# Kernel optimization log

Hardware: AMD Instinct MI355X
Metric: run time of the kernel (lower is better)

## Reference

```python
import jax, jax.numpy as jnp
import numpy as np

B, V, T = 8, 16, 64
DIN, H, RH, K, TMP = 6, 256, 64, 2, 256
E = V * (V - 1)
NREL, NPOS = 7, 3  # 2D relative / positional feature counts

_edges = np.ones((V, V)) - np.eye(V)
SEND = jnp.asarray(np.where(_edges)[0])
RECV = jnp.asarray(np.where(_edges)[1])


def _w(k, shape, fan):
    return jax.random.normal(k, shape, jnp.float32) / np.sqrt(fan)


def setup_inputs() -> dict:
    key = jax.random.key(0)
    ks = jax.random.split(key, 20)
    d = {}
    d['rel_feat'] = jax.random.normal(ks[0], (B, V, T, DIN), jnp.float32)
    d['edge_attr_raw'] = jax.random.normal(ks[1], (B, E, T, NREL + DIN), jnp.float32)
    d['edge_pos'] = jax.random.normal(ks[2], (B, E, T, NPOS), jnp.float32)
    d['ef_w1'] = _w(ks[3], (H, NREL + DIN + NPOS), NREL + DIN + NPOS); d['ef_b1'] = jnp.full((H,), 0.1)
    d['ef_w2'] = _w(ks[4], (H, H), H); d['ef_b2'] = jnp.full((H,), 0.1)
    d['res_w'] = _w(ks[5], (H, DIN), DIN); d['res_b'] = jnp.full((H,), 0.1)
    d['m3_w1'] = _w(ks[6], (H, H), H); d['m3_b1'] = jnp.full((H,), 0.1)
    d['m3_w2'] = _w(ks[7], (H, H), H); d['m3_b2'] = jnp.full((H,), 0.1)
    d['m4_w1'] = _w(ks[8], (H, 3 * H), 3 * H); d['m4_b1'] = jnp.full((H,), 0.1)
    d['m4_w2'] = _w(ks[9], (H, H), H); d['m4_b2'] = jnp.full((H,), 0.1)
    d['f_wih'] = _w(ks[10], (4 * RH, H), H); d['f_whh'] = _w(ks[11], (4 * RH, RH), RH)
    d['f_bih'] = jnp.zeros((4 * RH,)); d['f_bhh'] = jnp.zeros((4 * RH,))
    d['r_wih'] = _w(ks[12], (4 * RH, H), H); d['r_whh'] = _w(ks[13], (4 * RH, RH), RH)
    d['r_bih'] = jnp.zeros((4 * RH,)); d['r_bhh'] = jnp.zeros((4 * RH,))
    d['p_w'] = _w(ks[14], (K, RH), RH); d['p_b'] = jnp.full((K,), 0.1)
    d['e_w1'] = _w(ks[15], (TMP, 2 * RH), 2 * RH); d['e_b1'] = jnp.full((TMP,), 0.1)
    d['e_w2'] = _w(ks[16], (K, TMP), TMP); d['e_b2'] = jnp.full((K,), 0.1)
    return d


def _lstm(x, wih, whh, bih, bhh):
    # x: [N, T, H] -> hidden sequence [N, T, RH]; torch gate order i, f, g, o
    n = x.shape[0]
    rh = whh.shape[1]
    xw = jnp.einsum('nth,gh->ntg', x, wih) + bih  # input GEMM hoisted out of scan

    def step(carry, xt):
        h, c = carry
        z = xt + h @ whh.T + bhh
        i, f, g, o = jnp.split(z, 4, axis=-1)
        c = jax.nn.sigmoid(f) * c + jax.nn.sigmoid(i) * jnp.tanh(g)
        h = jax.nn.sigmoid(o) * jnp.tanh(c)
        return (h, c), h

    h0 = jnp.zeros((n, rh), x.dtype)
    _, hs = jax.lax.scan(step, (h0, h0), jnp.swapaxes(xw, 0, 1))
    return jnp.swapaxes(hs, 0, 1)


def reference(rel_feat, edge_attr_raw, edge_pos, ef_w1, ef_b1, ef_w2, ef_b2, res_w, res_b, m3_w1, m3_b1, m3_w2, m3_b2, m4_w1, m4_b1, m4_w2, m4_b2, f_wih, f_whh, f_bih, f_bhh, r_wih, r_whh, r_bih, r_bhh, p_w, p_b, e_w1, e_b1, e_w2, e_b2):
    elu = jax.nn.elu
    # edge filter MLP: [B,E,T,NREL+DIN+NPOS] -> [B,E,T,H]
    ein = jnp.concatenate([edge_attr_raw, edge_pos], -1)
    edge_attr = elu(elu(ein @ ef_w1.T + ef_b1) @ ef_w2.T + ef_b2)
    # edge2node: scatter-sum over recv indices, normalized by (V-1)
    agg = jax.ops.segment_sum(jnp.moveaxis(edge_attr, 1, 0), RECV, num_segments=V)
    x = jnp.moveaxis(agg, 0, 1) / (V - 1) + (rel_feat @ res_w.T + res_b)
    # mlp3 on node embeddings
    x = elu(elu(x @ m3_w1.T + m3_b1) @ m3_w2.T + m3_b2)
    # node2edge gather + skip-concat with previous edge features -> mlp4
    x = jnp.concatenate([x[:, SEND], x[:, RECV], edge_attr], -1)  # [B,E,T,3H]
    x = elu(elu(x @ m4_w1.T + m4_b1) @ m4_w2.T + m4_b2)  # [B,E,T,H]
    # bidirectional LSTM over time, per edge
    seq = x.reshape(B * E, T, H)
    fwd = _lstm(seq, f_wih, f_whh, f_bih, f_bhh)
    rev = jnp.flip(_lstm(jnp.flip(seq, 1), r_wih, r_whh, r_bih, r_bhh), 1)
    prior = (fwd @ p_w.T + p_b).reshape(B, E, T, K).transpose(0, 2, 1, 3)  # [B,T,E,K]
    comb = jnp.concatenate([fwd, rev], -1)
    enc = (elu(comb @ e_w1.T + e_b1) @ e_w2.T + e_b2).reshape(B, E, T, K).transpose(0, 2, 1, 3)
    return prior, enc
```

## Files before the change

kernel.cpp:

```cpp
#include <hip/hip_runtime.h>
#include <cstdint>
#include <cstddef>
#include <type_traits>

#define B_ 8
#define V_ 16
#define T_ 64
#define E_ 240
#define H_ 256
#define RH_ 64
#define K_ 2
#define DIN_ 6
#define BET_ (B_*E_*T_)
#define BVT_ (B_*V_*T_)
#define BE_ (B_*E_)

typedef unsigned short ushort_t;
typedef unsigned int u32;
typedef __attribute__((ext_vector_type(8))) short bf16x8;
typedef __attribute__((ext_vector_type(4))) float f32x4;

__device__ __forceinline__ float eluf(float x) { return x > 0.f ? x : __expf(x) - 1.f; }
__device__ __forceinline__ float fsig(float x) { return 1.f / (1.f + __expf(-x)); }
__device__ __forceinline__ float ftanh_(float x) {
    float y = fminf(fmaxf(x, -8.f), 8.f);
    float e = __expf(2.f * y);
    return (e - 1.f) / (e + 1.f);
}
__device__ __forceinline__ float b2f(ushort_t u) {
    union { float f; uint32_t i; } v; v.i = ((uint32_t)u) << 16; return v.f;
}
__device__ __forceinline__ ushort_t f2b(float f) {
    union { float f; uint32_t i; } v; v.f = f;
    uint32_t r = (v.i + 0x7FFFu + ((v.i >> 16) & 1u)) >> 16;
    return (ushort_t)r;
}

__device__ __forceinline__ void gll16(const void* g, void* l) {
    __builtin_amdgcn_global_load_lds(
        (const __attribute__((address_space(1))) u32*)g,
        (__attribute__((address_space(3))) u32*)l, 16, 0, 0);
}

template<int KD, int ACT>
__global__ __launch_bounds__(512, 2) void gemm8_k(
    const ushort_t* __restrict__ A, const ushort_t* __restrict__ Wt,
    const float* __restrict__ b1, const float* __restrict__ b2,
    ushort_t* __restrict__ C)
{
    __shared__ ushort_t lds[4][32][512];
    const int tid = threadIdx.x;
    const int lane = tid & 63;
    const int w = tid >> 6;
    const int wm = w >> 2, wn = w & 3;
    const int m0 = blockIdx.x * 256;
    const int r16 = lane & 15, kq = lane >> 4;
    constexpr int NH = KD / 32;

    const ushort_t* Ag0 = A + (size_t)(m0 + w * 16 + r16) * KD + kq * 8;
    const ushort_t* Ag1 = A + (size_t)(m0 + (w + 8) * 16 + r16) * KD + kq * 8;
    const ushort_t* Bg0 = Wt + (size_t)(w * 16 + r16) * KD + kq * 8;
    const ushort_t* Bg1 = Wt + (size_t)((w + 8) * 16 + r16) * KD + kq * 8;

    f32x4 acc[8][4];
    #pragma unroll
    for (int i = 0; i < 8; ++i)
        #pragma unroll
        for (int j = 0; j < 4; ++j)
            acc[i][j] = (f32x4){0.f, 0.f, 0.f, 0.f};

#define ST8(h) do { int sl_ = (h) & 3; int kk_ = (h) * 32;                  \
    gll16(Ag0 + kk_, &lds[sl_][w][0]);                                      \
    gll16(Ag1 + kk_, &lds[sl_][w + 8][0]);                                  \
    gll16(Bg0 + kk_, &lds[sl_][16 + w][0]);                                 \
    gll16(Bg1 + kk_, &lds[sl_][16 + w + 8][0]);                             \
} while (0)

    ST8(0); ST8(1); ST8(2);
    asm volatile("s_waitcnt vmcnt(8)" ::: "memory");
    __builtin_amdgcn_s_barrier();

    for (int h = 0; h < NH; ++h) {
        if (h + 3 < NH) ST8(h + 3);
        const int sl = h & 3;
        bf16x8 bfr[4];
        #pragma unroll
        for (int nf = 0; nf < 4; ++nf)
            bfr[nf] = *(const bf16x8*)&lds[sl][16 + wn * 4 + nf][lane * 8];
        #pragma unroll
        for (int mh = 0; mh < 2; ++mh) {
            bf16x8 af[4];
            #pragma unroll
            for (int mf = 0; mf < 4; ++mf)
                af[mf] = *(const bf16x8*)&lds[sl][wm * 8 + mh * 4 + mf][lane * 8];
            __builtin_amdgcn_s_setprio(1);
            #pragma unroll
            for (int mf = 0; mf < 4; ++mf)
                #pragma unroll
                for (int nf = 0; nf < 4; ++nf)
                    acc[mh * 4 + mf][nf] = __builtin_amdgcn_mfma_f32_16x16x32_bf16(
                        bfr[nf], af[mf], acc[mh * 4 + mf][nf], 0, 0, 0);
            __builtin_amdgcn_s_setprio(0);
        }
        asm volatile("s_waitcnt lgkmcnt(0)" ::: "memory");
        if (h < NH - 3)       { asm volatile("s_waitcnt vmcnt(8)" ::: "memory"); }
        else if (h == NH - 3) { asm volatile("s_waitcnt vmcnt(4)" ::: "memory"); }
        else if (h == NH - 2) { asm volatile("s_waitcnt vmcnt(0)" ::: "memory"); }
        if (h < NH - 1) __builtin_amdgcn_s_barrier();
    }
#undef ST8

    #pragma unroll
    for (int mi = 0; mi < 8; ++mi) {
        int mrow = m0 + wm * 128 + mi * 16 + r16;
        #pragma unroll
        for (int nf = 0; nf < 4; ++nf) {
            int nb = wn * 64 + nf * 16 + kq * 4;
            float4 bb = *(const float4*)&b1[nb];
            if (b2) {
                float4 b2v = *(const float4*)&b2[nb];
                bb.x += b2v.x; bb.y += b2v.y; bb.z += b2v.z; bb.w += b2v.w;
            }
            float v0 = acc[mi][nf][0] + bb.x;
            float v1 = acc[mi][nf][1] + bb.y;
            float v2 = acc[mi][nf][2] + bb.z;
            float v3 = acc[mi][nf][3] + bb.w;
            if (ACT) { v0 = eluf(v0); v1 = eluf(v1); v2 = eluf(v2); v3 = eluf(v3); }
            ushort4 o; o.x = f2b(v0); o.y = f2b(v1); o.z = f2b(v2); o.w = f2b(v3);
            *(ushort4*)&C[(size_t)mrow * 256 + nb] = o;
        }
    }
}

__global__ __launch_bounds__(512, 1) void gemm8_ef_k(
    const float* __restrict__ ear, const float* __restrict__ epos,
    const float* __restrict__ ef_w1, const float* __restrict__ ef_b1,
    const ushort_t* __restrict__ w_ef2, const float* __restrict__ ef_b2,
    ushort_t* __restrict__ EA)
{
    __shared__ ushort_t H1[8][8][512];
    __shared__ ushort_t slotB[4][16][512];
    const int tid = threadIdx.x;
    const int lane = tid & 63;
    const int w = tid >> 6;
    const int wm = w >> 2, wn = w & 3;
    const int m0 = blockIdx.x * 128;
    const int r16 = lane & 15, kq = lane >> 4;

    f32x4 acc[4][4];
    #pragma unroll
    for (int i = 0; i < 4; ++i)
        #pragma unroll
        for (int j = 0; j < 4; ++j)
            acc[i][j] = (f32x4){0.f, 0.f, 0.f, 0.f};
    {
        bf16x8 af[4], bfr[4];
        #pragma unroll
        for (int mf = 0; mf < 4; ++mf) {
            int m = m0 + wm * 64 + mf * 16 + r16;
            #pragma unroll
            for (int e = 0; e < 8; ++e) {
                float v = 0.f;
                if (kq < 2) {
                    int c = kq * 8 + e;
                    v = (c < 13) ? ear[(size_t)m * 13 + c] : epos[(size_t)m * 3 + (c - 13)];
                }
                af[mf][e] = (short)f2b(v);
            }
        }
        #pragma unroll
        for (int nf = 0; nf < 4; ++nf) {
            int n = wn * 64 + nf * 16 + r16;
            #pragma unroll
            for (int e = 0; e < 8; ++e) {
                float v = 0.f;
                if (kq < 2) v = ef_w1[(size_t)n * 16 + kq * 8 + e];
                bfr[nf][e] = (short)f2b(v);
            }
        }
        #pragma unroll
        for (int mf = 0; mf < 4; ++mf)
            #pragma unroll
            for (int nf = 0; nf < 4; ++nf)
                acc[mf][nf] = __builtin_amdgcn_mfma_f32_16x16x32_bf16(bfr[nf], af[mf], acc[mf][nf], 0, 0, 0);
    }

    const size_t bo0 = (size_t)(2 * w * 16 + r16) * 256 + kq * 8;
    const size_t bo1 = (size_t)((2 * w + 1) * 16 + r16) * 256 + kq * 8;
#define EF_ST(h) do { int sl_ = (h) & 3;                                    \
    gll16(w_ef2 + bo0 + (h) * 32, &slotB[sl_][2 * w][0]);                   \
    gll16(w_ef2 + bo1 + (h) * 32, &slotB[sl_][2 * w + 1][0]);               \
} while (0)

    EF_ST(0); EF_ST(1); EF_ST(2);

    #pragma unroll
    for (int mf = 0; mf < 4; ++mf) {
        #pragma unroll
        for (int nf = 0; nf < 4; ++nf) {
            int col = wn * 64 + nf * 16 + kq * 4;
            float4 bb = *(const float4*)&ef_b1[col];
            ushort4 o;
            o.x = f2b(eluf(acc[mf][nf][0] + bb.x));
            o.y = f2b(eluf(acc[mf][nf][1] + bb.y));
            o.z = f2b(eluf(acc[mf][nf][2] + bb.z));
            o.w = f2b(eluf(acc[mf][nf][3] + bb.w));
            int ktw = wn * 2 + (nf >> 1);
            int lanew = r16 + 16 * (((nf & 1) << 1) | (kq >> 1));
            *(ushort4*)&H1[wm * 4 + mf][ktw][lanew * 8 + (kq & 1) * 4] = o;
            acc[mf][nf] = (f32x4){0.f, 0.f, 0.f, 0.f};
        }
    }
    asm volatile("s_waitcnt lgkmcnt(0)" ::: "memory");
    asm volatile("s_waitcnt vmcnt(4)" ::: "memory");
    __builtin_amdgcn_s_barrier();

    #pragma unroll
    for (int h = 0; h < 8; ++h) {
        if (h + 3 < 8) EF_ST(h + 3);
        const int sl = h & 3;
        bf16x8 af[4], bfr[4];
        #pragma unroll
        for (int nf = 0; nf < 4; ++nf)
            bfr[nf] = *(const bf16x8*)&slotB[sl][wn * 4 + nf][lane * 8];
        #pragma unroll
        for (int mf = 0; mf < 4; ++mf)
            af[mf] = *(const bf16x8*)&H1[wm * 4 + mf][h][lane * 8];
        __builtin_amdgcn_s_setprio(1);
        #pragma unroll
        for (int mf = 0; mf < 4; ++mf)
            #pragma unroll
            for (int nf = 0; nf < 4; ++nf)
                acc[mf][nf] = __builtin_amdgcn_mfma_f32_16x16x32_bf16(bfr[nf], af[mf], acc[mf][nf], 0, 0, 0);
        __builtin_amdgcn_s_setprio(0);
        asm volatile("s_waitcnt lgkmcnt(0)" ::: "memory");
        if (h <= 4)      { asm volatile("s_waitcnt vmcnt(4)" ::: "memory"); }
        else if (h == 5) { asm volatile("s_waitcnt vmcnt(2)" ::: "memory"); }
        else if (h == 6) { asm volatile("s_waitcnt vmcnt(0)" ::: "memory"); }
        if (h < 7) __builtin_amdgcn_s_barrier();
    }
#undef EF_ST

    #pragma unroll
    for (int mf = 0; mf < 4; ++mf) {
        int row = m0 + wm * 64 + mf * 16 + r16;
        #pragma unroll
        for (int nf = 0; nf < 4; ++nf) {
            int col = wn * 64 + nf * 16 + kq * 4;
            float4 bb = *(const float4*)&ef_b2[col];
            ushort4 o;
            o.x = f2b(eluf(acc[mf][nf][0] + bb.x));
            o.y = f2b(eluf(acc[mf][nf][1] + bb.y));
            o.z = f2b(eluf(acc[mf][nf][2] + bb.z));
            o.w = f2b(eluf(acc[mf][nf][3] + bb.w));
            *(ushort4*)&EA[(size_t)row * 256 + col] = o;
        }
    }
}

__global__ __launch_bounds__(512, 1) void gemm8_mlp3_k(
    const ushort_t* __restrict__ Xb, const ushort_t* __restrict__ w1,
    const float* __restrict__ b1, const ushort_t* __restrict__ w2,
    const float* __restrict__ b2, ushort_t* __restrict__ Out)
{
    __shared__ ushort_t H1[8][8][512];
    __shared__ ushort_t slots[36864];
    const int tid = threadIdx.x;
    const int lane = tid & 63;
    const int w = tid >> 6;
    const int m0 = blockIdx.x * 128;
    const int r16 = lane & 15, kq = lane >> 4;

    const ushort_t* Ag = Xb + (size_t)(m0 + w * 16 + r16) * 256 + kq * 8;
    const size_t bo0 = (size_t)(2 * w * 16 + r16) * 256 + kq * 8;
    const size_t bo1 = (size_t)((2 * w + 1) * 16 + r16) * 256 + kq * 8;

    float4 bb1[2], bb2[2];
    #pragma unroll
    for (int nf = 0; nf < 2; ++nf) {
        bb1[nf] = *(const float4*)&b1[w * 32 + nf * 16 + kq * 4];
        bb2[nf] = *(const float4*)&b2[w * 32 + nf * 16 + kq * 4];
    }

#define M3_ST0(h) do { int sl_ = (h) % 3;                                   \
    gll16(Ag + (h) * 32, &slots[sl_ * 12288 + w * 512]);                    \
    gll16(w1 + bo0 + (h) * 32, &slots[sl_ * 12288 + 4096 + 2 * w * 512]);   \
    gll16(w1 + bo1 + (h) * 32, &slots[sl_ * 12288 + 4096 + (2 * w + 1) * 512]); \
} while (0)
#define M3_ST1(h) do { int sl_ = (h) & 1; int kk_ = (h) * 32;               \
    gll16(w2 + bo0 + kk_, &slots[sl_ * 8192 + 2 * w * 512]);                \
    gll16(w2 + bo1 + kk_, &slots[sl_ * 8192 + (2 * w + 1) * 512]);          \
} while (0)

    f32x4 acc0[8][2];
    #pragma unroll
    for (int i = 0; i < 8; ++i) { acc0[i][0] = (f32x4){0,0,0,0}; acc0[i][1] = (f32x4){0,0,0,0}; }

    M3_ST0(0); M3_ST0(1);
    asm volatile("s_waitcnt vmcnt(3)" ::: "memory");
    __builtin_amdgcn_s_barrier();

    for (int h = 0; h < 8; ++h) {
        if (h + 2 < 8) M3_ST0(h + 2);
        const int sl = h % 3;
        bf16x8 af[8], bfr[2];
        #pragma unroll
        for (int mf = 0; mf < 8; ++mf)
            af[mf] = *(const bf16x8*)&slots[sl * 12288 + mf * 512 + lane * 8];
        #pragma unroll
        for (int nf = 0; nf < 2; ++nf)
            bfr[nf] = *(const bf16x8*)&slots[sl * 12288 + 4096 + (2 * w + nf) * 512 + lane * 8];
        #pragma unroll
        for (int mf = 0; mf < 8; ++mf)
            #pragma unroll
            for (int nf = 0; nf < 2; ++nf)
                acc0[mf][nf] = __builtin_amdgcn_mfma_f32_16x16x32_bf16(bfr[nf], af[mf], acc0[mf][nf], 0, 0, 0);
        asm volatile("s_waitcnt lgkmcnt(0)" ::: "memory");
        if (h <= 5)      { asm volatile("s_waitcnt vmcnt(3)" ::: "memory"); }
        else if (h == 6) { asm volatile("s_waitcnt vmcnt(0)" ::: "memory"); }
        if (h < 7) __builtin_amdgcn_s_barrier();
    }

    M3_ST1(0);
    #pragma unroll
    for (int mf = 0; mf < 8; ++mf) {
        #pragma unroll
        for (int nf = 0; nf < 2; ++nf) {
            ushort4 o;
            o.x = f2b(eluf(acc0[mf][nf][0] + bb1[nf].x));
            o.y = f2b(eluf(acc0[mf][nf][1] + bb1[nf].y));
            o.z = f2b(eluf(acc0[mf][nf][2] + bb1[nf].z));
            o.w = f2b(eluf(acc0[mf][nf][3] + bb1[nf].w));
            int lanew = r16 + 16 * ((nf << 1) | (kq >> 1));
            *(ushort4*)&H1[mf][w][lanew * 8 + (kq & 1) * 4] = o;
            acc0[mf][nf] = (f32x4){0.f, 0.f, 0.f, 0.f};
        }
    }
    asm volatile("s_waitcnt lgkmcnt(0)" ::: "memory");
    asm volatile("s_waitcnt vmcnt(0)" ::: "memory");
    __builtin_amdgcn_s_barrier();

    for (int h = 0; h < 8; ++h) {
        if (h + 1 < 8) M3_ST1(h + 1);
        const int sl = h & 1;
        bf16x8 af[8], bfr[2];
        #pragma unroll
        for (int mf = 0; mf < 8; ++mf)
            af[mf] = *(const bf16x8*)&H1[mf][h][lane * 8];
        #pragma unroll
        for (int nf = 0; nf < 2; ++nf)
            bfr[nf] = *(const bf16x8*)&slots[sl * 8192 + (2 * w + nf) * 512 + lane * 8];
        #pragma unroll
        for (int mf = 0; mf < 8; ++mf)
            #pragma unroll
            for (int nf = 0; nf < 2; ++nf)
                acc0[mf][nf] = __builtin_amdgcn_mfma_f32_16x16x32_bf16(bfr[nf], af[mf], acc0[mf][nf], 0, 0, 0);
        asm volatile("s_waitcnt lgkmcnt(0)" ::: "memory");
        if (h + 1 < 8) { asm volatile("s_waitcnt vmcnt(0)" ::: "memory"); }
        if (h < 7) __builtin_amdgcn_s_barrier();
    }

    #pragma unroll
    for (int mf = 0; mf < 8; ++mf) {
        int row = m0 + mf * 16 + r16;
        #pragma unroll
        for (int nf = 0; nf < 2; ++nf) {
            int col = w * 32 + nf * 16 + kq * 4;
            ushort4 o;
            o.x = f2b(eluf(acc0[mf][nf][0] + bb2[nf].x));
            o.y = f2b(eluf(acc0[mf][nf][1] + bb2[nf].y));
            o.z = f2b(eluf(acc0[mf][nf][2] + bb2[nf].z));
            o.w = f2b(eluf(acc0[mf][nf][3] + bb2[nf].w));
            *(ushort4*)&Out[(size_t)row * 256 + col] = o;
        }
    }
#undef M3_ST0
#undef M3_ST1
}

__global__ __launch_bounds__(512, 2) void gemm8_mlp4_k(
    const ushort_t* __restrict__ X2b, const ushort_t* __restrict__ EA,
    const ushort_t* __restrict__ Wt, const float* __restrict__ b1,
    ushort_t* __restrict__ C)
{
    __shared__ ushort_t lds[4][32][512];
    const int tid = threadIdx.x;
    const int lane = tid & 63;
    const int w = tid >> 6;
    const int wm = w >> 2, wn = w & 3;
    const int m0 = blockIdx.x * 256;
    const int r16 = lane & 15, kq = lane >> 4;
    constexpr int NH = 24;

    const ushort_t* AS[2]; const ushort_t* AR[2]; const ushort_t* AE[2];
    #pragma unroll
    for (int ff = 0; ff < 2; ++ff) {
        int f = w + ff * 8;
        int m = m0 + f * 16 + r16;
        int be = m >> 6, t = m & 63;
        int b = be / E_, e = be % E_;
        int s = e / (V_ - 1);
        int r0 = e % (V_ - 1);
        int rr = r0 + (r0 >= s ? 1 : 0);
        AS[ff] = X2b + ((size_t)((b * V_ + s) * T_ + t)) * H_ + kq * 8;
        AR[ff] = X2b + ((size_t)((b * V_ + rr) * T_ + t)) * H_ + kq * 8;
        AE[ff] = EA + (size_t)m * H_ + kq * 8;
    }
    const ushort_t* Bg0 = Wt + (size_t)(w * 16 + r16) * 768 + kq * 8;
    const ushort_t* Bg1 = Wt + (size_t)((w + 8) * 16 + r16) * 768 + kq * 8;

    f32x4 acc[8][4];
    #pragma unroll
    for (int i = 0; i < 8; ++i)
        #pragma unroll
        for (int j = 0; j < 4; ++j)
            acc[i][j] = (f32x4){0.f, 0.f, 0.f, 0.f};

#define STM(h) do { int sl_ = (h) & 3; int kk_ = (h) * 32;                  \
    int seg_ = kk_ >> 8, off_ = kk_ & 255;                                  \
    const ushort_t* a0_ = (seg_ == 0 ? AS[0] : seg_ == 1 ? AR[0] : AE[0]) + off_; \
    const ushort_t* a1_ = (seg_ == 0 ? AS[1] : seg_ == 1 ? AR[1] : AE[1]) + off_; \
    gll16(a0_, &lds[sl_][w][0]);                                            \
    gll16(a1_, &lds[sl_][w + 8][0]);                                        \
    gll16(Bg0 + kk_, &lds[sl_][16 + w][0]);                                 \
    gll16(Bg1 + kk_, &lds[sl_][16 + w + 8][0]);                             \
} while (0)

    STM(0); STM(1); STM(2);
    asm volatile("s_waitcnt vmcnt(8)" ::: "memory");
    __builtin_amdgcn_s_barrier();

    for (int h = 0; h < NH; ++h) {
        if (h + 3 < NH) STM(h + 3);
        const int sl = h & 3;
        bf16x8 bfr[4];
        #pragma unroll
        for (int nf = 0; nf < 4; ++nf)
            bfr[nf] = *(const bf16x8*)&lds[sl][16 + wn * 4 + nf][lane * 8];
        #pragma unroll
        for (int mh = 0; mh < 2; ++mh) {
            bf16x8 af[4];
            #pragma unroll
            for (int mf = 0; mf < 4; ++mf)
                af[mf] = *(const bf16x8*)&lds[sl][wm * 8 + mh * 4 + mf][lane * 8];
            __builtin_amdgcn_s_setprio(1);
            #pragma unroll
            for (int mf = 0; mf < 4; ++mf)
                #pragma unroll
                for (int nf = 0; nf < 4; ++nf)
                    acc[mh * 4 + mf][nf] = __builtin_amdgcn_mfma_f32_16x16x32_bf16(
                        bfr[nf], af[mf], acc[mh * 4 + mf][nf], 0, 0, 0);
            __builtin_amdgcn_s_setprio(0);
        }
        asm volatile("s_waitcnt lgkmcnt(0)" ::: "memory");
        if (h < NH - 3)       { asm volatile("s_waitcnt vmcnt(8)" ::: "memory"); }
        else if (h == NH - 3) { asm volatile("s_waitcnt vmcnt(4)" ::: "memory"); }
        else if (h == NH - 2) { asm volatile("s_waitcnt vmcnt(0)" ::: "memory"); }
        if (h < NH - 1) __builtin_amdgcn_s_barrier();
    }
#undef STM

    #pragma unroll
    for (int mi = 0; mi < 8; ++mi) {
        int mrow = m0 + wm * 128 + mi * 16 + r16;
        #pragma unroll
        for (int nf = 0; nf < 4; ++nf) {
            int nb = wn * 64 + nf * 16 + kq * 4;
            float4 bb = *(const float4*)&b1[nb];
            float v0 = eluf(acc[mi][nf][0] + bb.x);
            float v1 = eluf(acc[mi][nf][1] + bb.y);
            float v2 = eluf(acc[mi][nf][2] + bb.z);
            float v3 = eluf(acc[mi][nf][3] + bb.w);
            ushort4 o; o.x = f2b(v0); o.y = f2b(v1); o.z = f2b(v2); o.w = f2b(v3);
            *(ushort4*)&C[(size_t)mrow * 256 + nb] = o;
        }
    }
}

__global__ __launch_bounds__(256) void wconv_k(
    const float* __restrict__ ef_w2, const float* __restrict__ m4_w1,
    const float* __restrict__ m4_w2, const float* __restrict__ f_wih,
    const float* __restrict__ r_wih, const float* __restrict__ e_w1,
    const float* __restrict__ m3_w1, const float* __restrict__ m3_w2,
    ushort_t* __restrict__ Wb)
{
    int i = blockIdx.x * 256 + threadIdx.x;
    const float* src; int off;
    if (i < 65536)       { src = ef_w2; off = i; }
    else if (i < 262144) { src = m4_w1; off = i - 65536; }
    else if (i < 327680) { src = m4_w2; off = i - 262144; }
    else if (i < 393216) { src = f_wih; off = i - 327680; }
    else if (i < 458752) { src = r_wih; off = i - 393216; }
    else if (i < 491520) { src = e_w1;  off = i - 458752; }
    else if (i < 557056) { src = m3_w1; off = i - 491520; }
    else                 { src = m3_w2; off = i - 557056; }
    Wb[i] = f2b(src[off]);
}

__global__ __launch_bounds__(256) void e2n_k(
    const ushort_t* __restrict__ EA, const float* __restrict__ rel,
    const float* __restrict__ res_w, const float* __restrict__ res_b,
    ushort_t* __restrict__ X)
{
    const int idx = blockIdx.x;
    const int t = idx & (T_ - 1);
    const int bv = idx >> 6;
    const int v = bv & (V_ - 1);
    const int b = bv >> 4;
    const int h = threadIdx.x;
    float sum = 0.f;
    #pragma unroll
    for (int i = 0; i < V_; ++i) {
        if (i == v) continue;
        int jj = (v < i) ? v : v - 1;
        int e = i * (V_ - 1) + jj;
        sum += b2f(EA[(((size_t)(b * E_ + e)) * T_ + t) * H_ + h]);
    }
    const float* rp = rel + ((size_t)bv * T_ + t) * DIN_;
    float res = res_b[h];
    #pragma unroll
    for (int d = 0; d < DIN_; ++d) res += rp[d] * res_w[h * DIN_ + d];
    X[((size_t)bv * T_ + t) * H_ + h] = f2b(sum * (1.f / 15.f) + res);
}

__global__ __launch_bounds__(256) void lstm_mfma4_k(
    const ushort_t* __restrict__ Gf, const ushort_t* __restrict__ Gr,
    const float* __restrict__ whh_f, const float* __restrict__ whh_r,
    ushort_t* __restrict__ COMB)
{
    __shared__ ushort_t hlds[2][1024];
    const int dir = blockIdx.y;
    const ushort_t* G = dir ? Gr : Gf;
    const float* whh = dir ? whh_r : whh_f;
    const int tid = threadIdx.x;
    const int lane = tid & 63;
    const int w = tid >> 6;
    const int seq = lane & 15, kq = lane >> 4;
    const int be0 = blockIdx.x * 16;
    const int swz = (seq & 7) << 4;

    bf16x8 wf[4][2];
    #pragma unroll
    for (int a = 0; a < 4; ++a) {
        #pragma unroll
        for (int ks = 0; ks < 2; ++ks) {
            const float* p = whh + (size_t)((a * 4 + w) * 16 + seq) * 64 + ks * 32 + kq * 8;
            float4 x0 = *(const float4*)p;
            float4 x1 = *(const float4*)(p + 4);
            bf16x8 v;
            v[0] = (short)f2b(x0.x); v[1] = (short)f2b(x0.y);
            v[2] = (short)f2b(x0.z); v[3] = (short)f2b(x0.w);
            v[4] = (short)f2b(x1.x); v[5] = (short)f2b(x1.y);
            v[6] = (short)f2b(x1.z); v[7] = (short)f2b(x1.w);
            wf[a][ks] = v;
        }
    }

    const ushort_t* grow = G + ((size_t)(be0 + seq) * T_) * 256 + kq * 4;
    ushort_t* crow = COMB + ((size_t)(be0 + seq) * T_) * 128 + (dir ? 64 : 0) + 16 * w + 4 * kq;

    float c[4] = {};
    ushort4 gx[4];
    const int t0 = dir ? (T_ - 1) : 0;
    #pragma unroll
    for (int a = 0; a < 4; ++a)
        gx[a] = *(const ushort4*)(grow + (size_t)t0 * 256 + (a * 4 + w) * 16);

    for (int s = 0; s < T_; ++s) {
        const int t = dir ? (T_ - 1 - s) : s;
        f32x4 acc[4];
        #pragma unroll
        for (int a = 0; a < 4; ++a) {
            ushort4 g = gx[a];
            acc[a] = (f32x4){b2f(g.x), b2f(g.y), b2f(g.z), b2f(g.w)};
        }
        if (s < T_ - 1) {
            const int tn = dir ? (T_ - 2 - s) : (s + 1);
            #pragma unroll
            for (int a = 0; a < 4; ++a)
                gx[a] = *(const ushort4*)(grow + (size_t)tn * 256 + (a * 4 + w) * 16);
        }
        if (s) {
            bf16x8 af[2];
            #pragma unroll
            for (int ks = 0; ks < 2; ++ks) {
                int boff = (seq * 128 + ks * 64 + kq * 16) ^ swz;
                af[ks] = *(const bf16x8*)((const char*)hlds[(s - 1) & 1] + boff);
            }
            #pragma unroll
            for (int a = 0; a < 4; ++a) {
                acc[a] = __builtin_amdgcn_mfma_f32_16x16x32_bf16(wf[a][0], af[0], acc[a], 0, 0, 0);
                acc[a] = __builtin_amdgcn_mfma_f32_16x16x32_bf16(wf[a][1], af[1], acc[a], 0, 0, 0);
            }
        }
        float hh[4];
        #pragma unroll
        for (int r = 0; r < 4; ++r) {
            float zi = acc[0][r], zf = acc[1][r], zg = acc[2][r], zo = acc[3][r];
            float cc = fsig(zf) * c[r] + fsig(zi) * ftanh_(zg);
            c[r] = cc;
            hh[r] = fsig(zo) * ftanh_(cc);
        }
        ushort4 hv;
        hv.x = f2b(hh[0]); hv.y = f2b(hh[1]); hv.z = f2b(hh[2]); hv.w = f2b(hh[3]);
        int wb = (seq * 128 + 32 * w + 8 * kq) ^ swz;
        *(ushort4*)((char*)hlds[s & 1] + wb) = hv;
        *(ushort4*)(crow + (size_t)t * 128) = hv;
        asm volatile("s_waitcnt lgkmcnt(0)" ::: "memory");
        __builtin_amdgcn_sched_barrier(0);
        __builtin_amdgcn_s_barrier();
    }
}

__global__ __launch_bounds__(256) void prior_k(
    const ushort_t* __restrict__ COMB, const float* __restrict__ p_w,
    const float* __restrict__ p_b, float* __restrict__ out)
{
    const int row = blockIdx.x * 4 + (threadIdx.x >> 6);
    const int lane = threadIdx.x & 63;
    float hf = b2f(COMB[(size_t)row * 128 + lane]);
    float v0 = hf * p_w[lane];
    float v1 = hf * p_w[64 + lane];
    #pragma unroll
    for (int off = 32; off > 0; off >>= 1) {
        v0 += __shfl_down(v0, off, 64);
        v1 += __shfl_down(v1, off, 64);
    }
    if (lane == 0) {
        int t = row & (T_ - 1);
        int be = row >> 6;
        int e = be % E_, b = be / E_;
        size_t o = (((size_t)b * T_ + t) * E_ + e) * K_;
        out[o] = v0 + p_b[0];
        out[o + 1] = v1 + p_b[1];
    }
}

__global__ __launch_bounds__(512) void fused_enc_k(
    const ushort_t* __restrict__ COMB, const ushort_t* __restrict__ w_e1,
    const float* __restrict__ e_b1, const float* __restrict__ e_w2,
    const float* __restrict__ e_b2, float* __restrict__ out)
{
    __shared__ ushort_t sA[2][8][512];
    __shared__ ushort_t sW[2][16][512];
    __shared__ float part[128][4][2];
    const int tid = threadIdx.x;
    const int lane = tid & 63;
    const int w = tid >> 6;
    const int wr = w >> 2, wc = w & 3;
    const int m0 = blockIdx.x * 128;
    const int r16 = lane & 15, kq = lane >> 4;

    const ushort_t* Asrc = COMB + (size_t)(m0 + w * 16 + r16) * 128 + kq * 8;
    const size_t woffA = (size_t)((2 * w) * 16 + r16) * 128 + kq * 8;
    const size_t woffB = (size_t)((2 * w + 1) * 16 + r16) * 128 + kq * 8;

    float4 w2v[2][4];
    #pragma unroll
    for (int j = 0; j < 2; ++j)
        #pragma unroll
        for (int nf = 0; nf < 4; ++nf)
            w2v[j][nf] = *(const float4*)&e_w2[j * 256 + wc * 64 + nf * 16 + kq * 4];

    f32x4 acc[4][4];
    #pragma unroll
    for (int i = 0; i < 4; ++i)
        #pragma unroll
        for (int j = 0; j < 4; ++j)
            acc[i][j] = (f32x4){0.f, 0.f, 0.f, 0.f};

#define FE_STAGE(bufi, kt_) do {                                             \
    gll16(Asrc + (kt_) * 32, &sA[bufi][w][0]);                               \
    gll16(w_e1 + woffA + (kt_) * 32, &sW[bufi][2 * w][0]);                   \
    gll16(w_e1 + woffB + (kt_) * 32, &sW[bufi][2 * w + 1][0]);               \
} while (0)

    FE_STAGE(0, 0);
    asm volatile("s_waitcnt vmcnt(0)" ::: "memory");
    __builtin_amdgcn_s_barrier();

    for (int s = 0; s < 4; ++s) {
        const int buf = s & 1;
        if (s < 3) FE_STAGE(buf ^ 1, s + 1);
        bf16x8 af[4], bfr[4];
        #pragma unroll
        for (int mf = 0; mf < 4; ++mf)
            af[mf] = *(const bf16x8*)&sA[buf][wr * 4 + mf][lane * 8];
        #pragma unroll
        for (int nf = 0; nf < 4; ++nf)
            bfr[nf] = *(const bf16x8*)&sW[buf][wc * 4 + nf][lane * 8];
        #pragma unroll
        for (int mf = 0; mf < 4; ++mf)
            #pragma unroll
            for (int nf = 0; nf < 4; ++nf)
                acc[mf][nf] = __builtin_amdgcn_mfma_f32_16x16x32_bf16(bfr[nf], af[mf], acc[mf][nf], 0, 0, 0);
        asm volatile("s_waitcnt vmcnt(0)" ::: "memory");
        __builtin_amdgcn_s_barrier();
    }

    #pragma unroll
    for (int mf = 0; mf < 4; ++mf) {
        float s0 = 0.f, s1 = 0.f;
        #pragma unroll
        for (int nf = 0; nf < 4; ++nf) {
            int col = wc * 64 + nf * 16 + kq * 4;
            float4 bb = *(const float4*)&e_b1[col];
            float v0 = eluf(acc[mf][nf][0] + bb.x);
            float v1 = eluf(acc[mf][nf][1] + bb.y);
            float v2 = eluf(acc[mf][nf][2] + bb.z);
            float v3 = eluf(acc[mf][nf][3] + bb.w);
            s0 += v0 * w2v[0][nf].x + v1 * w2v[0][nf].y + v2 * w2v[0][nf].z + v3 * w2v[0][nf].w;
            s1 += v0 * w2v[1][nf].x + v1 * w2v[1][nf].y + v2 * w2v[1][nf].z + v3 * w2v[1][nf].w;
        }
        s0 += __shfl_xor(s0, 16, 64); s0 += __shfl_xor(s0, 32, 64);
        s1 += __shfl_xor(s1, 16, 64); s1 += __shfl_xor(s1, 32, 64);
        if (kq == 0) {
            part[wr * 64 + mf * 16 + r16][wc][0] = s0;
            part[wr * 64 + mf * 16 + r16][wc][1] = s1;
        }
    }
    __syncthreads();
    if (tid < 256) {
        int row = tid >> 1, k = tid & 1;
        float v = part[row][0][k] + part[row][1][k] + part[row][2][k] + part[row][3][k] + e_b2[k];
        int gr = m0 + row;
        int be = gr >> 6, t = gr & 63;
        int e = be % E_, b = be / E_;
        out[(size_t)(B_ * T_ * E_ * K_) + (((size_t)b * T_ + t) * E_ + e) * K_ + k] = v;
    }
#undef FE_STAGE
}

extern "C" void kernel_launch(void* const* d_in, const int* in_sizes, int n_in,
                              void* d_out, int out_size, void* d_ws, size_t ws_size,
                              hipStream_t stream)
{
    const float* rel    = (const float*)d_in[0];
    const float* ear    = (const float*)d_in[1];
    const float* epos   = (const float*)d_in[2];
    const float* ef_w1  = (const float*)d_in[3];
    const float* ef_b1  = (const float*)d_in[4];
    const float* ef_w2  = (const float*)d_in[5];
    const float* ef_b2  = (const float*)d_in[6];
    const float* res_w  = (const float*)d_in[7];
    const float* res_b  = (const float*)d_in[8];
    const float* m3_w1  = (const float*)d_in[9];
    const float* m3_b1  = (const float*)d_in[10];
    const float* m3_w2  = (const float*)d_in[11];
    const float* m3_b2  = (const float*)d_in[12];
    const float* m4_w1  = (const float*)d_in[13];
    const float* m4_b1  = (const float*)d_in[14];
    const float* m4_w2  = (const float*)d_in[15];
    const float* m4_b2  = (const float*)d_in[16];
    const float* f_wih  = (const float*)d_in[17];
    const float* f_whh  = (const float*)d_in[18];
    const float* f_bih  = (const float*)d_in[19];
    const float* f_bhh  = (const float*)d_in[20];
    const float* r_wih  = (const float*)d_in[21];
    const float* r_whh  = (const float*)d_in[22];
    const float* r_bih  = (const float*)d_in[23];
    const float* r_bhh  = (const float*)d_in[24];
    const float* p_w    = (const float*)d_in[25];
    const float* p_b    = (const float*)d_in[26];
    const float* e_w1   = (const float*)d_in[27];
    const float* e_b1   = (const float*)d_in[28];
    const float* e_w2   = (const float*)d_in[29];
    const float* e_b2   = (const float*)d_in[30];
    float* out = (float*)d_out;

    char* ws = (char*)d_ws;
    const size_t BIGB  = (size_t)BET_ * H_ * sizeof(ushort_t);
    const size_t COMBB = (size_t)BET_ * 128 * sizeof(ushort_t);
    const size_t X2BB  = (size_t)BVT_ * H_ * sizeof(ushort_t);
    ushort_t* R1   = (ushort_t*)(ws);
    ushort_t* R2   = (ushort_t*)(ws + BIGB);
    ushort_t* COMB = (ushort_t*)(ws + 2 * BIGB);
    ushort_t* X2b  = (ushort_t*)(ws + 2 * BIGB + COMBB);
    ushort_t* Wb   = (ushort_t*)(ws + 2 * BIGB + COMBB + X2BB);
    ushort_t* Xbf = (ushort_t*)(ws);
    const ushort_t* wb_ef2  = Wb + 0;
    const ushort_t* wb_m41  = Wb + 65536;
    const ushort_t* wb_m42  = Wb + 262144;
    const ushort_t* wb_fwih = Wb + 327680;
    const ushort_t* wb_rwih = Wb + 393216;
    const ushort_t* wb_ew1  = Wb + 458752;
    const ushort_t* wb_m31  = Wb + 491520;
    const ushort_t* wb_m32  = Wb + 557056;

    dim3 blk(256);
    dim3 blk8(512);
    dim3 g128(BET_ / 128);
    dim3 g256(BET_ / 256);

    wconv_k<<<2432, blk, 0, stream>>>(ef_w2, m4_w1, m4_w2, f_wih, r_wih, e_w1, m3_w1, m3_w2, Wb);
    gemm8_ef_k<<<g128, blk8, 0, stream>>>(ear, epos, ef_w1, ef_b1, wb_ef2, ef_b2, R2);
    e2n_k<<<BVT_, blk, 0, stream>>>(R2, rel, res_w, res_b, Xbf);
    gemm8_mlp3_k<<<BVT_ / 128, blk8, 0, stream>>>(Xbf, wb_m31, m3_b1, wb_m32, m3_b2, X2b);
    gemm8_mlp4_k<<<g256, blk8, 0, stream>>>(X2b, R2, wb_m41, m4_b1, R1);
    gemm8_k<256, 1><<<g256, blk8, 0, stream>>>(R1, wb_m42, m4_b2, nullptr, R2);
    gemm8_k<256, 0><<<g256, blk8, 0, stream>>>(R2, wb_fwih, f_bih, f_bhh, R1);
    gemm8_k<256, 0><<<g256, blk8, 0, stream>>>(R2, wb_rwih, r_bih, r_bhh, R2);
    lstm_mfma4_k<<<dim3(BE_ / 16, 2), blk, 0, stream>>>(R1, R2, f_whh, r_whh, COMB);
    prior_k<<<BET_ / 4, blk, 0, stream>>>(COMB, p_w, p_b, out);
    fused_enc_k<<<g128, blk8, 0, stream>>>(COMB, wb_ew1, e_b1, e_w2, e_b2, out);
}
```

Measured before the change: 424.0 us.

## Split edge-filter MLP into two kernels and fuse forward/reverse LSTM input GEMMs

Replaces the fused two-layer edge-filter kernel with a small fp32 FMA GEMM for the K=16 first layer, which writes an intermediate to global memory. The generic bf16 MFMA GEMM kernel then runs the second layer from that intermediate. The two LSTM input-gate GEMMs are merged into one kernel: each 128-row A tile is loaded once, half the waves compute forward gates and half compute reverse gates, with a 3-slot pipelined LDS buffer. This removes one launch and a redundant read of the activations, but the edge-filter split adds a full write and read of a large intermediate tensor.

```diff
diff --git a/kernel.cpp b/kernel.cpp
--- a/kernel.cpp
+++ b/kernel.cpp
@@ -132,129 +132,144 @@
     }
 }
 
-__global__ __launch_bounds__(512, 1) void gemm8_ef_k(
-    const float* __restrict__ ear, const float* __restrict__ epos,
-    const float* __restrict__ ef_w1, const float* __restrict__ ef_b1,
-    const ushort_t* __restrict__ w_ef2, const float* __restrict__ ef_b2,
-    ushort_t* __restrict__ EA)
-{
-    __shared__ ushort_t H1[8][8][512];
-    __shared__ ushort_t slotB[4][16][512];
+__global__ __launch_bounds__(512, 1) void gemm8_gates_k(
+    const ushort_t* __restrict__ A, const ushort_t* __restrict__ w_fih,
+    const ushort_t* __restrict__ w_rih,
+    const float* __restrict__ f_bih, const float* __restrict__ f_bhh,
+    const float* __restrict__ r_bih, const float* __restrict__ r_bhh,
+    ushort_t* __restrict__ GF, ushort_t* __restrict__ GR)
+{
+    __shared__ ushort_t lds[3][40][512];
     const int tid = threadIdx.x;
     const int lane = tid & 63;
     const int w = tid >> 6;
-    const int wm = w >> 2, wn = w & 3;
     const int m0 = blockIdx.x * 128;
     const int r16 = lane & 15, kq = lane >> 4;
-
-    f32x4 acc[4][4];
-    #pragma unroll
-    for (int i = 0; i < 4; ++i)
+    constexpr int NH = 8;
+
+    const ushort_t* Ag = A + (size_t)(m0 + w * 16 + r16) * 256 + kq * 8;
+    const ushort_t* WB = (w < 4) ? w_fih : w_rih;
+    const int cb = (w & 3) * 64;
+
+    const float* bi = (w < 4) ? f_bih : r_bih;
+    const float* bh = (w < 4) ? f_bhh : r_bhh;
+    float4 bg[4];
+    #pragma unroll
+    for (int nf = 0; nf < 4; ++nf) {
+        int col = cb + nf * 16 + kq * 4;
+        float4 a = *(const float4*)&bi[col];
+        float4 b = *(const float4*)&bh[col];
+        bg[nf] = (float4){a.x + b.x, a.y + b.y, a.z + b.z, a.w + b.w};
+    }
+
+    f32x4 acc[8][4];
+    #pragma unroll
+    for (int i = 0; i < 8; ++i)
         #pragma unroll
         for (int j = 0; j < 4; ++j)
             acc[i][j] = (f32x4){0.f, 0.f, 0.f, 0.f};
-    {
-        bf16x8 af[4], bfr[4];
-        #pragma unroll
-        for (int mf = 0; mf < 4; ++mf) {
-            int m = m0 + wm * 64 + mf * 16 + r16;
-            #pragma unroll
-            for (int e = 0; e < 8; ++e) {
-                float v = 0.f;
-                if (kq < 2) {
-                    int c = kq * 8 + e;
-                    v = (c < 13) ? ear[(size_t)m * 13 + c] : epos[(size_t)m * 3 + (c - 13)];
-                }
-                af[mf][e] = (short)f2b(v);
-            }
-        }
+
+#define GST(h) do { int sl_ = (h) % 3; int kk_ = (h) * 32;                  \
+    gll16(Ag + kk_, &lds[sl_][w][0]);                                       \
+    _Pragma("unroll")                                                       \
+    for (int j = 0; j < 4; ++j)                                             \
+        gll16(WB + (size_t)(cb + j * 16 + r16) * 256 + kq * 8 + kk_,        \
+              &lds[sl_][8 + 4 * w + j][0]);                                 \
+} while (0)
+
+    GST(0); GST(1);
+    asm volatile("s_waitcnt vmcnt(5)" ::: "memory");
+    __builtin_amdgcn_s_barrier();
+
+    for (int h = 0; h < NH; ++h) {
+        if (h + 2 < NH) GST(h + 2);
+        const int sl = h % 3;
+        bf16x8 bfr[4];
+        #pragma unroll
+        for (int nf = 0; nf < 4; ++nf)
+            bfr[nf] = *(const bf16x8*)&lds[sl][8 + 4 * w + nf][lane * 8];
+        #pragma unroll
+        for (int mh = 0; mh < 2; ++mh) {
+            bf16x8 af[4];
+            #pragma unroll
+            for (int mf = 0; mf < 4; ++mf)
+                af[mf] = *(const bf16x8*)&lds[sl][mh * 4 + mf][lane * 8];
+            __builtin_amdgcn_s_setprio(1);
+            #pragma unroll
+            for (int mf = 0; mf < 4; ++mf)
+                #pragma unroll
+                for (int nf = 0; nf < 4; ++nf)
+                    acc[mh * 4 + mf][nf] = __builtin_amdgcn_mfma_f32_16x16x32_bf16(
+                        bfr[nf], af[mf], acc[mh * 4 + mf][nf], 0, 0, 0);
+            __builtin_amdgcn_s_setprio(0);
+        }
+        asm volatile("s_waitcnt lgkmcnt(0)" ::: "memory");
+        if (h <= NH - 3)      { asm volatile("s_waitcnt vmcnt(5)" ::: "memory"); }
+        else if (h == NH - 2) { asm volatile("s_waitcnt vmcnt(0)" ::: "memory"); }
+        if (h < NH - 1) __builtin_amdgcn_s_barrier();
+    }
+#undef GST
+
+    ushort_t* Wout = (w < 4) ? GF : GR;
+    #pragma unroll
+    for (int mi = 0; mi < 8; ++mi) {
+        int mrow = m0 + mi * 16 + r16;
         #pragma unroll
         for (int nf = 0; nf < 4; ++nf) {
-            int n = wn * 64 + nf * 16 + r16;
-            #pragma unroll
-            for (int e = 0; e < 8; ++e) {
-                float v = 0.f;
-                if (kq < 2) v = ef_w1[(size_t)n * 16 + kq * 8 + e];
-                bfr[nf][e] = (short)f2b(v);
-            }
-        }
-        #pragma unroll
-        for (int mf = 0; mf < 4; ++mf)
-            #pragma unroll
-            for (int nf = 0; nf < 4; ++nf)
-                acc[mf][nf] = __builtin_amdgcn_mfma_f32_16x16x32_bf16(bfr[nf], af[mf], acc[mf][nf], 0, 0, 0);
-    }
-
-    const size_t bo0 = (size_t)(2 * w * 16 + r16) * 256 + kq * 8;
-    const size_t bo1 = (size_t)((2 * w + 1) * 16 + r16) * 256 + kq * 8;
-#define EF_ST(h) do { int sl_ = (h) & 3;                                    \
-    gll16(w_ef2 + bo0 + (h) * 32, &slotB[sl_][2 * w][0]);                   \
-    gll16(w_ef2 + bo1 + (h) * 32, &slotB[sl_][2 * w + 1][0]);               \
-} while (0)
-
-    EF_ST(0); EF_ST(1); EF_ST(2);
-
-    #pragma unroll
-    for (int mf = 0; mf < 4; ++mf) {
-        #pragma unroll
-        for (int nf = 0; nf < 4; ++nf) {
-            int col = wn * 64 + nf * 16 + kq * 4;
-            float4 bb = *(const float4*)&ef_b1[col];
+            int col = cb + nf * 16 + kq * 4;
             ushort4 o;
-            o.x = f2b(eluf(acc[mf][nf][0] + bb.x));
-            o.y = f2b(eluf(acc[mf][nf][1] + bb.y));
-            o.z = f2b(eluf(acc[mf][nf][2] + bb.z));
-            o.w = f2b(eluf(acc[mf][nf][3] + bb.w));
-            int ktw = wn * 2 + (nf >> 1);
-            int lanew = r16 + 16 * (((nf & 1) << 1) | (kq >> 1));
-            *(ushort4*)&H1[wm * 4 + mf][ktw][lanew * 8 + (kq & 1) * 4] = o;
-            acc[mf][nf] = (f32x4){0.f, 0.f, 0.f, 0.f};
-        }
-    }
-    asm volatile("s_waitcnt lgkmcnt(0)" ::: "memory");
-    asm volatile("s_waitcnt vmcnt(4)" ::: "memory");
-    __builtin_amdgcn_s_barrier();
-
-    #pragma unroll
-    for (int h = 0; h < 8; ++h) {
-        if (h + 3 < 8) EF_ST(h + 3);
-        const int sl = h & 3;
-        bf16x8 af[4], bfr[4];
-        #pragma unroll
-        for (int nf = 0; nf < 4; ++nf)
-            bfr[nf] = *(const bf16x8*)&slotB[sl][wn * 4 + nf][lane * 8];
-        #pragma unroll
-        for (int mf = 0; mf < 4; ++mf)
-            af[mf] = *(const bf16x8*)&H1[wm * 4 + mf][h][lane * 8];
-        __builtin_amdgcn_s_setprio(1);
-        #pragma unroll
-        for (int mf = 0; mf < 4; ++mf)
-            #pragma unroll
-            for (int nf = 0; nf < 4; ++nf)
-                acc[mf][nf] = __builtin_amdgcn_mfma_f32_16x16x32_bf16(bfr[nf], af[mf], acc[mf][nf], 0, 0, 0);
-        __builtin_amdgcn_s_setprio(0);
-        asm volatile("s_waitcnt lgkmcnt(0)" ::: "memory");
-        if (h <= 4)      { asm volatile("s_waitcnt vmcnt(4)" ::: "memory"); }
-        else if (h == 5) { asm volatile("s_waitcnt vmcnt(2)" ::: "memory"); }
-        else if (h == 6) { asm volatile("s_waitcnt vmcnt(0)" ::: "memory"); }
-        if (h < 7) __builtin_amdgcn_s_barrier();
-    }
-#undef EF_ST
-
-    #pragma unroll
-    for (int mf = 0; mf < 4; ++mf) {
-        int row = m0 + wm * 64 + mf * 16 + r16;
-        #pragma unroll
-        for (int nf = 0; nf < 4; ++nf) {
-            int col = wn * 64 + nf * 16 + kq * 4;
-            float4 bb = *(const float4*)&ef_b2[col];
-            ushort4 o;
-            o.x = f2b(eluf(acc[mf][nf][0] + bb.x));
-            o.y = f2b(eluf(acc[mf][nf][1] + bb.y));
-            o.z = f2b(eluf(acc[mf][nf][2] + bb.z));
-            o.w = f2b(eluf(acc[mf][nf][3] + bb.w));
-            *(ushort4*)&EA[(size_t)row * 256 + col] = o;
-        }
+            o.x = f2b(acc[mi][nf][0] + bg[nf].x);
+            o.y = f2b(acc[mi][nf][1] + bg[nf].y);
+            o.z = f2b(acc[mi][nf][2] + bg[nf].z);
+            o.w = f2b(acc[mi][nf][3] + bg[nf].w);
+            *(ushort4*)&Wout[(size_t)mrow * 256 + col] = o;
+        }
+    }
+}
+
+__global__ __launch_bounds__(256) void gemm_ein_k(
+    const float* __restrict__ ear, const float* __restrict__ epos,
+    const float* __restrict__ W, const float* __restrict__ b1,
+    ushort_t* __restrict__ C)
+{
+    __shared__ float As[16][64];
+    __shared__ float Ws[16][64];
+    const int m0 = blockIdx.x * 64, n0 = blockIdx.y * 64;
+    const int tid = threadIdx.x;
+    const int tm = tid >> 4, tn = tid & 15;
+    const int lm = tid >> 2, lq = tid & 3;
+    const int m = m0 + lm;
+    float a_[4];
+    #pragma unroll
+    for (int q = 0; q < 4; ++q) {
+        int c = lq * 4 + q;
+        a_[q] = (c < 13) ? ear[(size_t)m * 13 + c] : epos[(size_t)m * 3 + (c - 13)];
+    }
+    float4 wv = *(const float4*)(W + (size_t)(n0 + lm) * 16 + lq * 4);
+    As[lq*4+0][lm] = a_[0]; As[lq*4+1][lm] = a_[1]; As[lq*4+2][lm] = a_[2]; As[lq*4+3][lm] = a_[3];
+    Ws[lq*4+0][lm] = wv.x; Ws[lq*4+1][lm] = wv.y; Ws[lq*4+2][lm] = wv.z; Ws[lq*4+3][lm] = wv.w;
+    __syncthreads();
+    float acc[4][4] = {};
+    #pragma unroll
+    for (int k = 0; k < 16; ++k) {
+        float4 a = *(const float4*)&As[k][tm * 4];
+        float4 w = *(const float4*)&Ws[k][tn * 4];
+        float aa[4] = {a.x, a.y, a.z, a.w};
+        float ww[4] = {w.x, w.y, w.z, w.w};
+        #pragma unroll
+        for (int i = 0; i < 4; ++i)
+            #pragma unroll
+            for (int j = 0; j < 4; ++j)
+                acc[i][j] += aa[i] * ww[j];
+    }
+    #pragma unroll
+    for (int i = 0; i < 4; ++i) {
+        ushort4 o;
+        o.x = f2b(eluf(acc[i][0] + b1[n0 + tn*4 + 0]));
+        o.y = f2b(eluf(acc[i][1] + b1[n0 + tn*4 + 1]));
+        o.z = f2b(eluf(acc[i][2] + b1[n0 + tn*4 + 2]));
+        o.w = f2b(eluf(acc[i][3] + b1[n0 + tn*4 + 3]));
+        *(ushort4*)(C + (size_t)(m0 + tm * 4 + i) * H_ + (n0 + tn * 4)) = o;
     }
 }
 
@@ -791,15 +806,17 @@
     dim3 blk8(512);
     dim3 g128(BET_ / 128);
     dim3 g256(BET_ / 256);
+    dim3 gE64(BET_ / 64, 4);
 
     wconv_k<<<2432, blk, 0, stream>>>(ef_w2, m4_w1, m4_w2, f_wih, r_wih, e_w1, m3_w1, m3_w2, Wb);
-    gemm8_ef_k<<<g128, blk8, 0, stream>>>(ear, epos, ef_w1, ef_b1, wb_ef2, ef_b2, R2);
+    gemm_ein_k<<<gE64, blk, 0, stream>>>(ear, epos, ef_w1, ef_b1, R1);
+    gemm8_k<256, 1><<<g256, blk8, 0, stream>>>(R1, wb_ef2, ef_b2, nullptr, R2);
     e2n_k<<<BVT_, blk, 0, stream>>>(R2, rel, res_w, res_b, Xbf);
     gemm8_mlp3_k<<<BVT_ / 128, blk8, 0, stream>>>(Xbf, wb_m31, m3_b1, wb_m32, m3_b2, X2b);
     gemm8_mlp4_k<<<g256, blk8, 0, stream>>>(X2b, R2, wb_m41, m4_b1, R1);
     gemm8_k<256, 1><<<g256, blk8, 0, stream>>>(R1, wb_m42, m4_b2, nullptr, R2);
-    gemm8_k<256, 0><<<g256, blk8, 0, stream>>>(R2, wb_fwih, f_bih, f_bhh, R1);
-    gemm8_k<256, 0><<<g256, blk8, 0, stream>>>(R2, wb_rwih, r_bih, r_bhh, R2);
+    gemm8_gates_k<<<g128, blk8, 0, stream>>>(R2, wb_fwih, wb_rwih,
+                                             f_bih, f_bhh, r_bih, r_bhh, R1, R2);
     lstm_mfma4_k<<<dim3(BE_ / 16, 2), blk, 0, stream>>>(R1, R2, f_whh, r_whh, COMB);
     prior_k<<<BET_ / 4, blk, 0, stream>>>(COMB, p_w, p_b, out);
     fused_enc_k<<<g128, blk8, 0, stream>>>(COMB, wb_ew1, e_b1, e_w2, e_b2, out);
```

Result: faster. 404.4 us (median of 3 runs) (-4.6%).
